# Performance work log

Hardware: AMD Instinct MI355X
Metric: run time of the kernel (lower is better)

Reference implementation:

```python
import jax, jax.numpy as jnp
import numpy as np

NUM_FIELDS = 40
EMBED_DIM = 64
IN_SUB = 40
OUT_SUB = 40
BATCH = 256


def setup_inputs() -> dict:
    key = jax.random.key(0)
    k0, k1 = jax.random.split(key)
    B0 = jax.random.normal(k0, (BATCH, NUM_FIELDS, EMBED_DIM), dtype=jnp.float32)
    Bi = jax.random.normal(k1, (BATCH, IN_SUB, EMBED_DIM), dtype=jnp.float32)
    # parameters, initialized exactly as in the torch module
    W = jnp.tile(jnp.eye(EMBED_DIM, dtype=jnp.float32)[None], (OUT_SUB, 1, 1))  # (n, D, D)
    alpha = jnp.ones((NUM_FIELDS, IN_SUB, OUT_SUB), dtype=jnp.float32)          # (f, i, n)
    h = jnp.ones((OUT_SUB, EMBED_DIM, 1), dtype=jnp.float32)                    # (n, D, 1)
    return {"B0": B0, "Bi": Bi, "W": W, "alpha": alpha, "h": h}


def reference(B0, Bi, W, alpha, h):
    # Math of the original: fusion[b,n,D,d] = sum_{f,i} B0[b,f,D]*Bi[b,i,d]*alpha[f,i,n]
    # (equivalent to the 5D outer product contracted with alpha, but never
    #  materializes the (b,f,i,D,D) tensor).
    fusion = jnp.einsum('bfD,bid,fin->bnDd', B0, Bi, alpha)  # (b, n, D, D)
    # elementwise scale by W then project with h: out[b,n,D] = sum_d fusion*W*h
    out = jnp.einsum('bnDd,nDd,nd->bnD', fusion, W, h[..., 0])
    return out
```

## Files before the change

kernel.cpp:

```cpp
#include <hip/hip_runtime.h>
#include <hip/hip_bf16.h>

#define NF 40
#define NI 40
#define NN 40
#define ED 64
#define NB 256

typedef __attribute__((ext_vector_type(8))) short   short8;
typedef __attribute__((ext_vector_type(8))) __bf16  bf16x8;
typedef __attribute__((ext_vector_type(4))) float   f32x4;

__device__ __forceinline__ unsigned short f2bf(float x) {
    union { float f; unsigned u; } v; v.f = x;
    unsigned r = v.u + 0x7FFFu + ((v.u >> 16) & 1u);
    return (unsigned short)(r >> 16);
}

__device__ __forceinline__ bf16x8 ld_frag(const unsigned short* p) {
    return __builtin_bit_cast(bf16x8, *(const short8*)p);
}

__device__ __forceinline__ f32x4 mfma16(bf16x8 a, bf16x8 b, f32x4 c) {
    return __builtin_amdgcn_mfma_f32_16x16x32_bf16(a, b, c, 0, 0, 0);
}

#define BIP_N (48 * 64)
#define B0T_N (64 * 64)
#define WHP_N (64 * 64)
#define ALP_N (48 * 64)

__global__ __launch_bounds__(256) void gif_prep3(
        const float* __restrict__ B0, const float* __restrict__ Bi,
        const float* __restrict__ W, const float* __restrict__ alpha,
        const float* __restrict__ h,
        unsigned short* __restrict__ BiP, unsigned short* __restrict__ B0T,
        unsigned short* __restrict__ whp, unsigned short* __restrict__ alp) {
    const int x = blockIdx.x;
    const int t = threadIdx.x;

    if (x < NB) {
        const int b = x;
        __shared__ float sB0[NF][ED + 1];
        for (int idx = t; idx < NF * ED; idx += 256) {
            int f = idx >> 6, D = idx & 63;
            sB0[f][D] = B0[b * NF * ED + idx];
        }
        __syncthreads();
        for (int idx = t; idx < 48 * 64; idx += 256) {
            int i = idx >> 6, d = idx & 63;
            BiP[b * BIP_N + idx] = (i < NI) ? f2bf(Bi[b * NI * ED + i * ED + d])
                                            : (unsigned short)0;
        }
        for (int idx = t; idx < 64 * 64; idx += 256) {
            int D = idx >> 6, f = idx & 63;
            B0T[b * B0T_N + idx] = (f < NF) ? f2bf(sB0[f][D]) : (unsigned short)0;
        }
    } else if (x < NB + NN) {
        const int n = x - NB;
        for (int idx = t; idx < 64 * 64; idx += 256) {
            int d = idx & 63;
            whp[n * WHP_N + idx] = f2bf(W[n * ED * ED + idx] * h[n * ED + d]);
        }
        for (int idx = t; idx < 48 * 64; idx += 256) {
            int i = idx >> 6, f = idx & 63;
            if (i >= NI || f >= NF) alp[n * ALP_N + idx] = 0;
        }
    } else {
        const int f = x - NB - NN;
        for (int idx = t; idx < NI * NN; idx += 256) {
            int i = idx / NN, n = idx - i * NN;
            alp[n * ALP_N + i * 64 + f] = f2bf(alpha[(f * NI + i) * NN + n]);
        }
    }
}

__global__ __launch_bounds__(512, 2) void gif_main3(
        const unsigned short* __restrict__ BiP,
        const unsigned short* __restrict__ B0T,
        const unsigned short* __restrict__ whp,
        const unsigned short* __restrict__ alp,
        float* __restrict__ out) {
    const int b = blockIdx.x;
    const int t = threadIdx.x;
    const int lane = t & 63, w = t >> 6;
    const int quad = lane >> 4, l15 = lane & 15, fo = quad * 8;

    const unsigned short* bip = BiP + b * BIP_N;
    const unsigned short* b0t = B0T + b * B0T_N;

    bf16x8 biA[3][2], b0B[4][2];
#pragma unroll
    for (int m = 0; m < 3; ++m)
#pragma unroll
        for (int s = 0; s < 2; ++s)
            biA[m][s] = ld_frag(&bip[(m * 16 + l15) * 64 + s * 32 + fo]);
#pragma unroll
    for (int tt = 0; tt < 4; ++tt)
#pragma unroll
        for (int s = 0; s < 2; ++s)
            b0B[tt][s] = ld_frag(&b0t[(tt * 16 + l15) * 64 + s * 32 + fo]);

    bf16x8 alA[2][3][2], whB[2][4][2];
    {
        const unsigned short* ap = alp + w * ALP_N;
        const unsigned short* wp = whp + w * WHP_N;
#pragma unroll
        for (int m = 0; m < 3; ++m)
#pragma unroll
            for (int s = 0; s < 2; ++s)
                alA[0][m][s] = ld_frag(&ap[(m * 16 + l15) * 64 + s * 32 + fo]);
#pragma unroll
        for (int tt = 0; tt < 4; ++tt)
#pragma unroll
            for (int s = 0; s < 2; ++s)
                whB[0][tt][s] = ld_frag(&wp[(tt * 16 + l15) * 64 + s * 32 + fo]);
    }

#pragma unroll
    for (int it = 0; it < 5; ++it) {
        const int cur = it & 1, nxt = cur ^ 1;
        const int n = w + 8 * it;

        if (it < 4) {
            const unsigned short* ap = alp + (n + 8) * ALP_N;
            const unsigned short* wp = whp + (n + 8) * WHP_N;
#pragma unroll
            for (int m = 0; m < 3; ++m)
#pragma unroll
                for (int s = 0; s < 2; ++s)
                    alA[nxt][m][s] = ld_frag(&ap[(m * 16 + l15) * 64 + s * 32 + fo]);
#pragma unroll
            for (int tt = 0; tt < 4; ++tt)
#pragma unroll
                for (int s = 0; s < 2; ++s)
                    whB[nxt][tt][s] = ld_frag(&wp[(tt * 16 + l15) * 64 + s * 32 + fo]);
        }

        float p[4];
#pragma unroll
        for (int tt = 0; tt < 4; ++tt) {
            float acc = 0.f;
#pragma unroll
            for (int m = 0; m < 3; ++m) {
                f32x4 z = {0.f, 0.f, 0.f, 0.f};
                f32x4 T = mfma16(biA[m][0], whB[cur][tt][0], z);
                T = mfma16(biA[m][1], whB[cur][tt][1], T);
                f32x4 G = mfma16(alA[cur][m][0], b0B[tt][0], z);
                G = mfma16(alA[cur][m][1], b0B[tt][1], G);
                acc += T[0] * G[0] + T[1] * G[1] + T[2] * G[2] + T[3] * G[3];
            }
            p[tt] = acc;
        }
#pragma unroll
        for (int tt = 0; tt < 4; ++tt) {
            p[tt] += __shfl_xor(p[tt], 16, 64);
            p[tt] += __shfl_xor(p[tt], 32, 64);
        }
        float v = (quad == 0) ? p[0] : (quad == 1) ? p[1] : (quad == 2) ? p[2] : p[3];
        out[(b * NN + n) * ED + lane] = v;
    }
}

#define PS 72
#define WH_N (ED * PS)
#define AL_N (48 * PS)

__global__ __launch_bounds__(256) void gif_prep(
        const float* __restrict__ W, const float* __restrict__ alpha,
        const float* __restrict__ h,
        unsigned short* __restrict__ whp, unsigned short* __restrict__ alp) {
    const int n = blockIdx.x;
    const int t0 = blockIdx.y * 256 + threadIdx.x;
    for (int idx = t0; idx < ED * PS; idx += 1024) {
        int D = idx / PS, c = idx - D * PS;
        float v = (c < ED) ? W[n * ED * ED + D * ED + c] * h[n * ED + c] : 0.f;
        whp[n * WH_N + idx] = f2bf(v);
    }
    for (int idx = t0; idx < 48 * PS; idx += 1024) {
        int i = idx / PS, c = idx - i * PS;
        float v = (i < NI && c < NF) ? alpha[(c * NI + i) * NN + n] : 0.f;
        alp[n * AL_N + idx] = f2bf(v);
    }
}

__device__ __forceinline__ bf16x8 mk_al_frag(const float* __restrict__ alpha,
        int n, int m, int s, int l15, int quad) {
    bf16x8 r;
    const int row = m * 16 + l15;
    const int f0 = s * 32 + quad * 8;
#pragma unroll
    for (int j = 0; j < 8; ++j) {
        const int f = f0 + j;
        float v = (row < NI && f < NF) ? alpha[(f * NI + row) * NN + n] : 0.f;
        r[j] = (__bf16)v;
    }
    return r;
}
__device__ __forceinline__ bf16x8 mk_wh_frag(const float* __restrict__ W,
        const float* __restrict__ h, int n, int tt, int s, int l15, int quad) {
    bf16x8 r;
    const int row = tt * 16 + l15;
    const int k0 = s * 32 + quad * 8;
#pragma unroll
    for (int j = 0; j < 8; ++j) {
        float v = W[n * ED * ED + row * ED + k0 + j] * h[n * ED + k0 + j];
        r[j] = (__bf16)v;
    }
    return r;
}

__global__ __launch_bounds__(256) void gif_mfma(
        const float* __restrict__ B0, const float* __restrict__ Bi,
        const unsigned short* __restrict__ whp, const unsigned short* __restrict__ alp,
        const float* __restrict__ W, const float* __restrict__ alpha,
        const float* __restrict__ h, int useWs, float* __restrict__ out) {
    const int q = blockIdx.x >> 8;
    const int b = blockIdx.x & 255;

    __shared__ __align__(16) unsigned short sBi[48 * PS];
    __shared__ __align__(16) unsigned short sBT[ED * PS];

    const int t = threadIdx.x;
    for (int idx = t; idx < 48 * PS; idx += 256) {
        int i = idx / PS, c = idx - i * PS;
        sBi[idx] = (i < NI && c < ED) ? f2bf(Bi[b * NI * ED + i * ED + c])
                                      : (unsigned short)0;
    }
    for (int idx = t; idx < ED * PS; idx += 256) {
        int D = idx / PS, c = idx - D * PS;
        sBT[idx] = (c < NF) ? f2bf(B0[b * NF * ED + c * ED + D])
                            : (unsigned short)0;
    }
    __syncthreads();

    const int lane = t & 63, w = t >> 6;
    const int quad = lane >> 4, l15 = lane & 15;
    const int fragoff = quad * 8;

    bf16x8 biA[3][2], b0B[4][2];
#pragma unroll
    for (int m = 0; m < 3; ++m)
#pragma unroll
        for (int s = 0; s < 2; ++s)
            biA[m][s] = ld_frag(&sBi[(m * 16 + l15) * PS + s * 32 + fragoff]);
#pragma unroll
    for (int tt = 0; tt < 4; ++tt)
#pragma unroll
        for (int s = 0; s < 2; ++s)
            b0B[tt][s] = ld_frag(&sBT[(tt * 16 + l15) * PS + s * 32 + fragoff]);

#pragma unroll
    for (int rep = 0; rep < 2; ++rep) {
        const int n = q * 8 + w + rep * 4;

        bf16x8 alA[3][2];
        if (useWs) {
#pragma unroll
            for (int m = 0; m < 3; ++m)
#pragma unroll
                for (int s = 0; s < 2; ++s)
                    alA[m][s] = ld_frag(&alp[n * AL_N + (m * 16 + l15) * PS + s * 32 + fragoff]);
        } else {
#pragma unroll
            for (int m = 0; m < 3; ++m)
#pragma unroll
                for (int s = 0; s < 2; ++s)
                    alA[m][s] = mk_al_frag(alpha, n, m, s, l15, quad);
        }

        float p[4];
#pragma unroll
        for (int tt = 0; tt < 4; ++tt) {
            bf16x8 whB[2];
            if (useWs) {
                const unsigned short* wpp = &whp[n * WH_N + (tt * 16 + l15) * PS + fragoff];
                whB[0] = ld_frag(wpp);
                whB[1] = ld_frag(wpp + 32);
            } else {
                whB[0] = mk_wh_frag(W, h, n, tt, 0, l15, quad);
                whB[1] = mk_wh_frag(W, h, n, tt, 1, l15, quad);
            }
            float acc = 0.f;
#pragma unroll
            for (int m = 0; m < 3; ++m) {
                f32x4 z = {0.f, 0.f, 0.f, 0.f};
                f32x4 T = mfma16(biA[m][0], whB[0], z);
                T = mfma16(biA[m][1], whB[1], T);
                f32x4 G = mfma16(alA[m][0], b0B[tt][0], z);
                G = mfma16(alA[m][1], b0B[tt][1], G);
                acc += T[0] * G[0] + T[1] * G[1] + T[2] * G[2] + T[3] * G[3];
            }
            p[tt] = acc;
        }
#pragma unroll
        for (int tt = 0; tt < 4; ++tt) {
            p[tt] += __shfl_xor(p[tt], 16, 64);
            p[tt] += __shfl_xor(p[tt], 32, 64);
        }
        float v = (quad == 0) ? p[0] : (quad == 1) ? p[1] : (quad == 2) ? p[2] : p[3];
        out[(b * NN + n) * ED + lane] = v;
    }
}

extern "C" void kernel_launch(void* const* d_in, const int* in_sizes, int n_in,
                              void* d_out, int out_size, void* d_ws, size_t ws_size,
                              hipStream_t stream) {
    const float* B0    = (const float*)d_in[0];
    const float* Bi    = (const float*)d_in[1];
    const float* W     = (const float*)d_in[2];
    const float* alpha = (const float*)d_in[3];
    const float* h     = (const float*)d_in[4];
    float* out = (float*)d_out;

    const size_t need2 =
        (size_t)(NB * BIP_N + NB * B0T_N + NN * WHP_N + NN * ALP_N) * sizeof(unsigned short);
    if (ws_size >= need2) {
        unsigned short* BiP = (unsigned short*)d_ws;
        unsigned short* B0T = BiP + (size_t)NB * BIP_N;
        unsigned short* whp = B0T + (size_t)NB * B0T_N;
        unsigned short* alp = whp + (size_t)NN * WHP_N;
        gif_prep3<<<NB + NN + NF, 256, 0, stream>>>(B0, Bi, W, alpha, h, BiP, B0T, whp, alp);
        gif_main3<<<NB, 512, 0, stream>>>(BiP, B0T, whp, alp, out);
        return;
    }

    const size_t need1 = (size_t)(NN * WH_N + NN * AL_N) * sizeof(unsigned short);
    const int useWs = (ws_size >= need1) ? 1 : 0;
    unsigned short* whp = (unsigned short*)d_ws;
    unsigned short* alp = whp + (size_t)NN * WH_N;
    if (useWs) {
        gif_prep<<<dim3(NN, 4), 256, 0, stream>>>(W, alpha, h, whp, alp);
    }
    gif_mfma<<<5 * NB, 256, 0, stream>>>(B0, Bi, whp, alp, W, alpha, h, useWs, out);
}
```

Baseline: 92.49 us.

## Fuse per-batch bf16 conversion into main kernel via LDS and split outputs across two blocks

Moves the per-batch conversion of B0 and Bi to bf16 (and the transpose of B0) out of the prep kernel into the main kernel, staging them in padded shared memory instead of writing and re-reading packed workspace buffers in global memory. The main kernel now launches 512 blocks of 256 threads, with each block handling half of the 40 output subspaces for one batch, instead of 256 blocks of 512 threads. This removes a global round trip for the activations and shrinks the prep kernel. In exchange, each batch's inputs are loaded and converted twice, and each block adds an LDS staging step with a barrier.

```diff
diff --git a/kernel.cpp b/kernel.cpp
--- a/kernel.cpp
+++ b/kernel.cpp
@@ -25,49 +25,29 @@
     return __builtin_amdgcn_mfma_f32_16x16x32_bf16(a, b, c, 0, 0, 0);
 }
 
-#define BIP_N (48 * 64)
-#define B0T_N (64 * 64)
 #define WHP_N (64 * 64)
 #define ALP_N (48 * 64)
 
-__global__ __launch_bounds__(256) void gif_prep3(
-        const float* __restrict__ B0, const float* __restrict__ Bi,
+__global__ __launch_bounds__(256) void gif_prep4(
         const float* __restrict__ W, const float* __restrict__ alpha,
         const float* __restrict__ h,
-        unsigned short* __restrict__ BiP, unsigned short* __restrict__ B0T,
         unsigned short* __restrict__ whp, unsigned short* __restrict__ alp) {
     const int x = blockIdx.x;
     const int t = threadIdx.x;
-
-    if (x < NB) {
-        const int b = x;
-        __shared__ float sB0[NF][ED + 1];
-        for (int idx = t; idx < NF * ED; idx += 256) {
-            int f = idx >> 6, D = idx & 63;
-            sB0[f][D] = B0[b * NF * ED + idx];
-        }
-        __syncthreads();
-        for (int idx = t; idx < 48 * 64; idx += 256) {
-            int i = idx >> 6, d = idx & 63;
-            BiP[b * BIP_N + idx] = (i < NI) ? f2bf(Bi[b * NI * ED + i * ED + d])
-                                            : (unsigned short)0;
-        }
-        for (int idx = t; idx < 64 * 64; idx += 256) {
-            int D = idx >> 6, f = idx & 63;
-            B0T[b * B0T_N + idx] = (f < NF) ? f2bf(sB0[f][D]) : (unsigned short)0;
-        }
-    } else if (x < NB + NN) {
-        const int n = x - NB;
+    if (x < NN) {
+        const int n = x;
         for (int idx = t; idx < 64 * 64; idx += 256) {
             int d = idx & 63;
             whp[n * WHP_N + idx] = f2bf(W[n * ED * ED + idx] * h[n * ED + d]);
         }
-        for (int idx = t; idx < 48 * 64; idx += 256) {
-            int i = idx >> 6, f = idx & 63;
-            if (i >= NI || f >= NF) alp[n * ALP_N + idx] = 0;
+        for (int idx = t; idx < 8 * 64; idx += 256)
+            alp[n * ALP_N + (40 + (idx >> 6)) * 64 + (idx & 63)] = 0;
+        for (int idx = t; idx < 40 * 24; idx += 256) {
+            int i = idx / 24, f = 40 + idx - i * 24;
+            alp[n * ALP_N + i * 64 + f] = 0;
         }
     } else {
-        const int f = x - NB - NN;
+        const int f = x - NN;
         for (int idx = t; idx < NI * NN; idx += 256) {
             int i = idx / NN, n = idx - i * NN;
             alp[n * ALP_N + i * 64 + f] = f2bf(alpha[(f * NI + i) * NN + n]);
@@ -75,36 +55,26 @@
     }
 }
 
-__global__ __launch_bounds__(512, 2) void gif_main3(
-        const unsigned short* __restrict__ BiP,
-        const unsigned short* __restrict__ B0T,
+#define PSM 72
+__global__ __launch_bounds__(256, 2) void gif_main4(
+        const float* __restrict__ B0, const float* __restrict__ Bi,
         const unsigned short* __restrict__ whp,
         const unsigned short* __restrict__ alp,
         float* __restrict__ out) {
-    const int b = blockIdx.x;
+    const int q = blockIdx.x >> 8;
+    const int b = blockIdx.x & 255;
     const int t = threadIdx.x;
     const int lane = t & 63, w = t >> 6;
     const int quad = lane >> 4, l15 = lane & 15, fo = quad * 8;
 
-    const unsigned short* bip = BiP + b * BIP_N;
-    const unsigned short* b0t = B0T + b * B0T_N;
-
-    bf16x8 biA[3][2], b0B[4][2];
-#pragma unroll
-    for (int m = 0; m < 3; ++m)
-#pragma unroll
-        for (int s = 0; s < 2; ++s)
-            biA[m][s] = ld_frag(&bip[(m * 16 + l15) * 64 + s * 32 + fo]);
-#pragma unroll
-    for (int tt = 0; tt < 4; ++tt)
-#pragma unroll
-        for (int s = 0; s < 2; ++s)
-            b0B[tt][s] = ld_frag(&b0t[(tt * 16 + l15) * 64 + s * 32 + fo]);
+    __shared__ __align__(16) unsigned short sBi[48 * PSM];
+    __shared__ __align__(16) unsigned short sBT[64 * PSM];
 
     bf16x8 alA[2][3][2], whB[2][4][2];
     {
-        const unsigned short* ap = alp + w * ALP_N;
-        const unsigned short* wp = whp + w * WHP_N;
+        const int n0 = q * 20 + w;
+        const unsigned short* ap = alp + n0 * ALP_N;
+        const unsigned short* wp = whp + n0 * WHP_N;
 #pragma unroll
         for (int m = 0; m < 3; ++m)
 #pragma unroll
@@ -117,14 +87,46 @@
                 whB[0][tt][s] = ld_frag(&wp[(tt * 16 + l15) * 64 + s * 32 + fo]);
     }
 
+    {
+        const float* bi = Bi + b * NI * ED;
+        const float* b0 = B0 + b * NF * ED;
+        for (int idx = t; idx < NI * ED; idx += 256) {
+            int i = idx >> 6, d = idx & 63;
+            sBi[i * PSM + d] = f2bf(bi[idx]);
+        }
+        for (int idx = t; idx < 8 * 64; idx += 256)
+            sBi[(40 + (idx >> 6)) * PSM + (idx & 63)] = 0;
+        for (int idx = t; idx < NF * ED; idx += 256) {
+            int f = idx >> 6, D = idx & 63;
+            sBT[D * PSM + f] = f2bf(b0[idx]);
+        }
+        for (int idx = t; idx < 64 * 24; idx += 256) {
+            int D = idx / 24, f = 40 + idx - D * 24;
+            sBT[D * PSM + f] = 0;
+        }
+    }
+    __syncthreads();
+
+    bf16x8 biA[3][2], b0B[4][2];
+#pragma unroll
+    for (int m = 0; m < 3; ++m)
+#pragma unroll
+        for (int s = 0; s < 2; ++s)
+            biA[m][s] = ld_frag(&sBi[(m * 16 + l15) * PSM + s * 32 + fo]);
+#pragma unroll
+    for (int tt = 0; tt < 4; ++tt)
+#pragma unroll
+        for (int s = 0; s < 2; ++s)
+            b0B[tt][s] = ld_frag(&sBT[(tt * 16 + l15) * PSM + s * 32 + fo]);
+
 #pragma unroll
     for (int it = 0; it < 5; ++it) {
         const int cur = it & 1, nxt = cur ^ 1;
-        const int n = w + 8 * it;
+        const int n = q * 20 + it * 4 + w;
 
         if (it < 4) {
-            const unsigned short* ap = alp + (n + 8) * ALP_N;
-            const unsigned short* wp = whp + (n + 8) * WHP_N;
+            const unsigned short* ap = alp + (n + 4) * ALP_N;
+            const unsigned short* wp = whp + (n + 4) * WHP_N;
 #pragma unroll
             for (int m = 0; m < 3; ++m)
 #pragma unroll
@@ -313,15 +315,12 @@
     const float* h     = (const float*)d_in[4];
     float* out = (float*)d_out;
 
-    const size_t need2 =
-        (size_t)(NB * BIP_N + NB * B0T_N + NN * WHP_N + NN * ALP_N) * sizeof(unsigned short);
+    const size_t need2 = (size_t)(NN * WHP_N + NN * ALP_N) * sizeof(unsigned short);
     if (ws_size >= need2) {
-        unsigned short* BiP = (unsigned short*)d_ws;
-        unsigned short* B0T = BiP + (size_t)NB * BIP_N;
-        unsigned short* whp = B0T + (size_t)NB * B0T_N;
+        unsigned short* whp = (unsigned short*)d_ws;
         unsigned short* alp = whp + (size_t)NN * WHP_N;
-        gif_prep3<<<NB + NN + NF, 256, 0, stream>>>(B0, Bi, W, alpha, h, BiP, B0T, whp, alp);
-        gif_main3<<<NB, 512, 0, stream>>>(BiP, B0T, whp, alp, out);
+        gif_prep4<<<NN + NF, 256, 0, stream>>>(W, alpha, h, whp, alp);
+        gif_main4<<<2 * NB, 256, 0, stream>>>(B0, Bi, whp, alp, out);
         return;
     }
 
```

Measured after the change: 89.00 us. -3.8%, faster.

## Keep n-weights in registers and stream batch tiles through double-buffered LDS

Applied to the files above, without the earlier changes.

The main kernel's work split changes. Previously each block handled one batch element and looped over all 40 n values, reloading alpha and W*h fragments from global memory. Now each block fixes 4 n values, keeps their alpha and W*h fragments in registers, and loops over 8 batch elements. The Bi and B0 tiles for those elements are double-buffered through padded LDS, with register prefetch of the next tile. The prep kernel also zeroes only the padding region of alp. The trade-off is more, smaller blocks (320) plus a __syncthreads per batch step and LDS staging, in exchange for reusing the weight fragments across batch elements.

```diff
diff --git a/kernel.cpp b/kernel.cpp
--- a/kernel.cpp
+++ b/kernel.cpp
@@ -30,7 +30,7 @@
 #define WHP_N (64 * 64)
 #define ALP_N (48 * 64)
 
-__global__ __launch_bounds__(256) void gif_prep3(
+__global__ __launch_bounds__(256) void gif_prep5(
         const float* __restrict__ B0, const float* __restrict__ Bi,
         const float* __restrict__ W, const float* __restrict__ alpha,
         const float* __restrict__ h,
@@ -62,9 +62,11 @@
             int d = idx & 63;
             whp[n * WHP_N + idx] = f2bf(W[n * ED * ED + idx] * h[n * ED + d]);
         }
-        for (int idx = t; idx < 48 * 64; idx += 256) {
-            int i = idx >> 6, f = idx & 63;
-            if (i >= NI || f >= NF) alp[n * ALP_N + idx] = 0;
+        for (int idx = t; idx < 8 * 64; idx += 256)
+            alp[n * ALP_N + (40 + (idx >> 6)) * 64 + (idx & 63)] = 0;
+        for (int idx = t; idx < 40 * 24; idx += 256) {
+            int i = idx / 24, f = 40 + idx - i * 24;
+            alp[n * ALP_N + i * 64 + f] = 0;
         }
     } else {
         const int f = x - NB - NN;
@@ -75,79 +77,101 @@
     }
 }
 
-__global__ __launch_bounds__(512, 2) void gif_main3(
+#define PSM 72
+#define LBI (48 * PSM)
+#define LBUF (LBI + 64 * PSM)
+#define NCHUNK 896
+
+__global__ __launch_bounds__(256, 2) void gif_main5(
         const unsigned short* __restrict__ BiP,
         const unsigned short* __restrict__ B0T,
         const unsigned short* __restrict__ whp,
         const unsigned short* __restrict__ alp,
         float* __restrict__ out) {
-    const int b = blockIdx.x;
+    const int bg = blockIdx.x;
+    const int ng = blockIdx.y;
     const int t = threadIdx.x;
     const int lane = t & 63, w = t >> 6;
     const int quad = lane >> 4, l15 = lane & 15, fo = quad * 8;
-
-    const unsigned short* bip = BiP + b * BIP_N;
-    const unsigned short* b0t = B0T + b * B0T_N;
-
-    bf16x8 biA[3][2], b0B[4][2];
-#pragma unroll
-    for (int m = 0; m < 3; ++m)
-#pragma unroll
-        for (int s = 0; s < 2; ++s)
-            biA[m][s] = ld_frag(&bip[(m * 16 + l15) * 64 + s * 32 + fo]);
-#pragma unroll
-    for (int tt = 0; tt < 4; ++tt)
-#pragma unroll
-        for (int s = 0; s < 2; ++s)
-            b0B[tt][s] = ld_frag(&b0t[(tt * 16 + l15) * 64 + s * 32 + fo]);
-
-    bf16x8 alA[2][3][2], whB[2][4][2];
+    const int n = ng * 4 + w;
+
+    __shared__ __align__(16) unsigned short sBuf[2 * LBUF];
+
+    bf16x8 alA[3][2], whB[4][2];
     {
-        const unsigned short* ap = alp + w * ALP_N;
-        const unsigned short* wp = whp + w * WHP_N;
+        const unsigned short* ap = alp + n * ALP_N;
+        const unsigned short* wp = whp + n * WHP_N;
 #pragma unroll
         for (int m = 0; m < 3; ++m)
 #pragma unroll
             for (int s = 0; s < 2; ++s)
-                alA[0][m][s] = ld_frag(&ap[(m * 16 + l15) * 64 + s * 32 + fo]);
+                alA[m][s] = ld_frag(&ap[(m * 16 + l15) * 64 + s * 32 + fo]);
 #pragma unroll
         for (int tt = 0; tt < 4; ++tt)
 #pragma unroll
             for (int s = 0; s < 2; ++s)
-                whB[0][tt][s] = ld_frag(&wp[(tt * 16 + l15) * 64 + s * 32 + fo]);
-    }
-
-#pragma unroll
-    for (int it = 0; it < 5; ++it) {
-        const int cur = it & 1, nxt = cur ^ 1;
-        const int n = w + 8 * it;
-
-        if (it < 4) {
-            const unsigned short* ap = alp + (n + 8) * ALP_N;
-            const unsigned short* wp = whp + (n + 8) * WHP_N;
-#pragma unroll
-            for (int m = 0; m < 3; ++m)
-#pragma unroll
-                for (int s = 0; s < 2; ++s)
-                    alA[nxt][m][s] = ld_frag(&ap[(m * 16 + l15) * 64 + s * 32 + fo]);
-#pragma unroll
-            for (int tt = 0; tt < 4; ++tt)
-#pragma unroll
-                for (int s = 0; s < 2; ++s)
-                    whB[nxt][tt][s] = ld_frag(&wp[(tt * 16 + l15) * 64 + s * 32 + fo]);
-        }
+                whB[tt][s] = ld_frag(&wp[(tt * 16 + l15) * 64 + s * 32 + fo]);
+    }
+
+    float4 creg[4];
+    {
+        const float4* sBi = (const float4*)(BiP + (size_t)(bg * 8) * BIP_N);
+        const float4* sB0 = (const float4*)(B0T + (size_t)(bg * 8) * B0T_N);
+#pragma unroll
+        for (int k = 0; k < 4; ++k) {
+            int c = t + k * 256;
+            if (c < NCHUNK) creg[k] = (c < 384) ? sBi[c] : sB0[c - 384];
+        }
+#pragma unroll
+        for (int k = 0; k < 4; ++k) {
+            int c = t + k * 256;
+            if (c < NCHUNK) {
+                int dst = (c < 384)
+                    ? ((c >> 3) * PSM + (c & 7) * 8)
+                    : (LBI + (((c - 384) >> 3) * PSM + ((c - 384) & 7) * 8));
+                *(float4*)&sBuf[dst] = creg[k];
+            }
+        }
+    }
+    __syncthreads();
+
+#pragma unroll 2
+    for (int j = 0; j < 8; ++j) {
+        const int b = bg * 8 + j;
+        const int cur = j & 1;
+
+        if (j < 7) {
+            const float4* sBi = (const float4*)(BiP + (size_t)(b + 1) * BIP_N);
+            const float4* sB0 = (const float4*)(B0T + (size_t)(b + 1) * B0T_N);
+#pragma unroll
+            for (int k = 0; k < 4; ++k) {
+                int c = t + k * 256;
+                if (c < NCHUNK) creg[k] = (c < 384) ? sBi[c] : sB0[c - 384];
+            }
+        }
+
+        const unsigned short* sbi = sBuf + cur * LBUF;
+        const unsigned short* sbt = sbi + LBI;
+        bf16x8 biA[3][2];
+#pragma unroll
+        for (int m = 0; m < 3; ++m)
+#pragma unroll
+            for (int s = 0; s < 2; ++s)
+                biA[m][s] = ld_frag(&sbi[(m * 16 + l15) * PSM + s * 32 + fo]);
 
         float p[4];
 #pragma unroll
         for (int tt = 0; tt < 4; ++tt) {
+            bf16x8 bb0 = ld_frag(&sbt[(tt * 16 + l15) * PSM + fo]);
+            bf16x8 bb1 = ld_frag(&sbt[(tt * 16 + l15) * PSM + 32 + fo]);
             float acc = 0.f;
 #pragma unroll
             for (int m = 0; m < 3; ++m) {
                 f32x4 z = {0.f, 0.f, 0.f, 0.f};
-                f32x4 T = mfma16(biA[m][0], whB[cur][tt][0], z);
-                T = mfma16(biA[m][1], whB[cur][tt][1], T);
-                f32x4 G = mfma16(alA[cur][m][0], b0B[tt][0], z);
-                G = mfma16(alA[cur][m][1], b0B[tt][1], G);
+                f32x4 T = mfma16(biA[m][0], whB[tt][0], z);
+                T = mfma16(biA[m][1], whB[tt][1], T);
+                f32x4 G = mfma16(alA[m][0], bb0, z);
+                G = mfma16(alA[m][1], bb1, G);
                 acc += T[0] * G[0] + T[1] * G[1] + T[2] * G[2] + T[3] * G[3];
             }
             p[tt] = acc;
@@ -159,6 +183,21 @@
         }
         float v = (quad == 0) ? p[0] : (quad == 1) ? p[1] : (quad == 2) ? p[2] : p[3];
         out[(b * NN + n) * ED + lane] = v;
+
+        if (j < 7) {
+            const int nb = cur ^ 1;
+#pragma unroll
+            for (int k = 0; k < 4; ++k) {
+                int c = t + k * 256;
+                if (c < NCHUNK) {
+                    int dst = (c < 384)
+                        ? ((c >> 3) * PSM + (c & 7) * 8)
+                        : (LBI + (((c - 384) >> 3) * PSM + ((c - 384) & 7) * 8));
+                    *(float4*)&sBuf[nb * LBUF + dst] = creg[k];
+                }
+            }
+        }
+        __syncthreads();
     }
 }
 
@@ -272,21 +311,21 @@
         float p[4];
 #pragma unroll
         for (int tt = 0; tt < 4; ++tt) {
-            bf16x8 whB[2];
+            bf16x8 whB2[2];
             if (useWs) {
                 const unsigned short* wpp = &whp[n * WH_N + (tt * 16 + l15) * PS + fragoff];
-                whB[0] = ld_frag(wpp);
-                whB[1] = ld_frag(wpp + 32);
+                whB2[0] = ld_frag(wpp);
+                whB2[1] = ld_frag(wpp + 32);
             } else {
-                whB[0] = mk_wh_frag(W, h, n, tt, 0, l15, quad);
-                whB[1] = mk_wh_frag(W, h, n, tt, 1, l15, quad);
+                whB2[0] = mk_wh_frag(W, h, n, tt, 0, l15, quad);
+                whB2[1] = mk_wh_frag(W, h, n, tt, 1, l15, quad);
             }
             float acc = 0.f;
 #pragma unroll
             for (int m = 0; m < 3; ++m) {
                 f32x4 z = {0.f, 0.f, 0.f, 0.f};
-                f32x4 T = mfma16(biA[m][0], whB[0], z);
-                T = mfma16(biA[m][1], whB[1], T);
+                f32x4 T = mfma16(biA[m][0], whB2[0], z);
+                T = mfma16(biA[m][1], whB2[1], T);
                 f32x4 G = mfma16(alA[m][0], b0B[tt][0], z);
                 G = mfma16(alA[m][1], b0B[tt][1], G);
                 acc += T[0] * G[0] + T[1] * G[1] + T[2] * G[2] + T[3] * G[3];
@@ -320,8 +359,8 @@
         unsigned short* B0T = BiP + (size_t)NB * BIP_N;
         unsigned short* whp = B0T + (size_t)NB * B0T_N;
         unsigned short* alp = whp + (size_t)NN * WHP_N;
-        gif_prep3<<<NB + NN + NF, 256, 0, stream>>>(B0, Bi, W, alpha, h, BiP, B0T, whp, alp);
-        gif_main3<<<NB, 512, 0, stream>>>(BiP, B0T, whp, alp, out);
+        gif_prep5<<<NB + NN + NF, 256, 0, stream>>>(B0, Bi, W, alpha, h, BiP, B0T, whp, alp);
+        gif_main5<<<dim3(32, 10), 256, 0, stream>>>(BiP, B0T, whp, alp, out);
         return;
     }
 
```

Result: slower. 99.89 us (+8.0%).
